# Kernel tuning notes

Measured on AMD Instinct MI355X. Metric: run time of the kernel, lower is better.

The kernel has to match this reference:

```python
import jax, jax.numpy as jnp
import numpy as np
from jax import lax

EPS = 1e-5
TRUNK_C, REG_C, GPOOL_C = 256, 192, 64
B, H, W = 256, 19, 19


def setup_inputs() -> dict:
    key = jax.random.key(0)
    ks = jax.random.split(key, 18)
    def bn_params(k, c):
        k1, k2, k3, k4 = jax.random.split(k, 4)
        return (jax.random.normal(k1, (c,)) * 0.1 + 1.0,   # gamma
                jax.random.normal(k2, (c,)) * 0.1,          # beta
                jax.random.normal(k3, (c,)) * 0.1,          # running mean
                jax.random.uniform(k4, (c,)) * 0.5 + 0.5)   # running var
    bn1_g, bn1_b, bn1_m, bn1_v = bn_params(ks[0], TRUNK_C)
    bn1b_g, bn1b_b, bn1b_m, bn1b_v = bn_params(ks[1], GPOOL_C)
    bn2_g, bn2_b, bn2_m, bn2_v = bn_params(ks[2], REG_C)
    x = jax.random.normal(ks[3], (B, TRUNK_C, H, W), dtype=jnp.float32)
    w1a = jax.random.normal(ks[4], (REG_C, TRUNK_C, 3, 3), dtype=jnp.float32) * (1.0 / np.sqrt(TRUNK_C * 9))
    w1b = jax.random.normal(ks[5], (GPOOL_C, TRUNK_C, 3, 3), dtype=jnp.float32) * (1.0 / np.sqrt(TRUNK_C * 9))
    w_lin = jax.random.normal(ks[6], (REG_C, 3 * GPOOL_C), dtype=jnp.float32) * (1.0 / np.sqrt(3 * GPOOL_C))
    w2 = jax.random.normal(ks[7], (TRUNK_C, REG_C, 3, 3), dtype=jnp.float32) * (1.0 / np.sqrt(REG_C * 9))
    return {
        'x': x, 'bn1_g': bn1_g, 'bn1_b': bn1_b, 'bn1_m': bn1_m, 'bn1_v': bn1_v,
        'w1a': w1a, 'w1b': w1b,
        'bn1b_g': bn1b_g, 'bn1b_b': bn1b_b, 'bn1b_m': bn1b_m, 'bn1b_v': bn1b_v,
        'w_lin': w_lin,
        'bn2_g': bn2_g, 'bn2_b': bn2_b, 'bn2_m': bn2_m, 'bn2_v': bn2_v,
        'w2': w2,
    }


def _bn(x, g, b, m, v):
    # inference batchnorm over channel dim of NCHW
    inv = g / jnp.sqrt(v + EPS)
    return (x - m[:, None, None]) * inv[:, None, None] + b[:, None, None]


def _mish(x):
    return x * jnp.tanh(jax.nn.softplus(x))


def _conv(x, w):
    return lax.conv_general_dilated(x, w, (1, 1), 'SAME',
                                    dimension_numbers=('NCHW', 'OIHW', 'NCHW'))


def _kata_gpool(x):
    # x: [B, C, H, W] -> [B, 3C]: mean, mean*(sqrt(N)-14)/10, max
    b, c, h, w = x.shape
    n = float(h * w)
    sqrt_n = n ** 0.5
    mean = jnp.sum(x, axis=(2, 3)) / n
    max_val = jnp.max(x, axis=(2, 3))
    scaled_mean = mean * ((sqrt_n - 14.0) / 10.0)
    return jnp.concatenate([mean, scaled_mean, max_val], axis=1)


def reference(x, bn1_g, bn1_b, bn1_m, bn1_v, w1a, w1b,
              bn1b_g, bn1b_b, bn1b_m, bn1b_v, w_lin,
              bn2_g, bn2_b, bn2_m, bn2_v, w2):
    out = _mish(_bn(x, bn1_g, bn1_b, bn1_m, bn1_v))
    reg = _conv(out, w1a)                       # [B, REG_C, H, W]
    gp = _conv(out, w1b)                        # [B, GPOOL_C, H, W]
    gp = _mish(_bn(gp, bn1b_g, bn1b_b, bn1b_m, bn1b_v))
    gp_pooled = _kata_gpool(gp)                 # [B, 3*GPOOL_C]
    gp_out = gp_pooled @ w_lin.T                # [B, REG_C]
    reg = reg + gp_out[:, :, None, None]
    out2 = _mish(_bn(reg, bn2_g, bn2_b, bn2_m, bn2_v))
    out2 = _conv(out2, w2)
    return out2 + x
```

## Files before the change

kernel.cpp:

```cpp
#include <hip/hip_runtime.h>
#include <hip/hip_bf16.h>
#include <math.h>


#define BATCH   256
#define TRUNK_C 256
#define REG_C   192
#define GPOOL_C 64
#define HH      19
#define WW      19
#define HW      361
#define PP      441
#define EPS     1e-5f

typedef __hip_bfloat16 bf16;
typedef __attribute__((ext_vector_type(8))) short short8;
typedef __attribute__((ext_vector_type(4))) float floatx4;

__device__ __forceinline__ float b2f(bf16 v) { return __bfloat162float(v); }
__device__ __forceinline__ bf16  f2b(float v) { return __float2bfloat16(v); }

__device__ __forceinline__ float mish_f(float v) {
    if (v > 20.0f) return v;
    float u = __expf(v);
    float n = u * (u + 2.0f);
    return v * __fdividef(n, n + 2.0f);
}

__device__ __forceinline__ void gload_lds16(const void* gsrc, void* lds) {
    __builtin_amdgcn_global_load_lds(
        (const __attribute__((address_space(1))) void*)gsrc,
        (__attribute__((address_space(3))) void*)lds, 16, 0, 0);
}

__global__ void prep_kernel(
    const float* g1, const float* b1, const float* m1, const float* v1,
    const float* g1b, const float* b1b, const float* m1b, const float* v1b,
    const float* g2, const float* b2, const float* m2, const float* v2,
    const float* __restrict__ w1a, const float* __restrict__ w1b,
    const float* __restrict__ w2,
    bf16* __restrict__ w1c_p, bf16* __restrict__ w2_p,
    bf16* __restrict__ act_pad, bf16* __restrict__ reg_pad,
    float* bnbuf)
{
    const int T1  = 16 * 72 * 64 * 8;
    const int T2  = 16 * 54 * 64 * 8;
    const int TW  = T1 + T2;
    const int TBa = BATCH * 80 * 32;
    const int TBr = BATCH * 80 * 24;
    int i = blockIdx.x * blockDim.x + threadIdx.x;
    if (i < TW) {
        if (i < T1) {
            int j = i & 7, lane = (i >> 3) & 63;
            int kc = (i >> 9) % 72, cog = (i >> 9) / 72;
            int co = cog * 16 + (lane & 15);
            int k = kc * 32 + ((lane >> 4) << 3) + j;
            int r = k >> 8, ci = k & 255;
            float v = (co < 192) ? w1a[co * 2304 + ci * 9 + r]
                                 : w1b[(co - 192) * 2304 + ci * 9 + r];
            w1c_p[i] = f2b(v);
        } else {
            int i2 = i - T1;
            int j = i2 & 7, lane = (i2 >> 3) & 63;
            int kc = (i2 >> 9) % 54, cog = (i2 >> 9) / 54;
            int co = cog * 16 + (lane & 15);
            int k = kc * 32 + ((lane >> 4) << 3) + j;
            int r = k / 192, ci = k % 192;
            w2_p[i2] = f2b(w2[co * 1728 + ci * 9 + r]);
        }
    } else if (i < TW + TBa + TBr) {
        int j = i - TW;
        bool isact = j < TBa;
        if (!isact) j -= TBa;
        int nb = isact ? 32 : 24;
        int b = j / (80 * nb);
        int rem = j - b * (80 * nb);
        int e = rem / nb, g = rem - (rem / nb) * nb;
        int pp;
        if (e < 21) pp = e;
        else if (e < 42) pp = 420 + (e - 21);
        else if (e < 61) pp = (e - 41) * 21;
        else pp = (e - 60) * 21 + 20;
        short8 z = {0, 0, 0, 0, 0, 0, 0, 0};
        if (isact) *(short8*)(act_pad + ((size_t)b * PP + pp) * TRUNK_C + g * 8) = z;
        else       *(short8*)(reg_pad + ((size_t)b * PP + pp) * REG_C + g * 8) = z;
    } else {
        int t = i - (TW + TBa + TBr);
        if (t < 256) {
            float s = g1[t] / sqrtf(v1[t] + EPS);
            bnbuf[t] = s;
            bnbuf[256 + t] = b1[t] - m1[t] * s;
        } else if (t < 320) {
            int c = t - 256;
            float s = g1b[c] / sqrtf(v1b[c] + EPS);
            bnbuf[512 + c] = s;
            bnbuf[576 + c] = b1b[c] - m1b[c] * s;
        } else if (t < 512) {
            int c = t - 320;
            float s = g2[c] / sqrtf(v2[c] + EPS);
            bnbuf[640 + c] = s;
            bnbuf[832 + c] = b2[c] - m2[c] * s;
        }
    }
}

__global__ __launch_bounds__(256)
void bn1_mish_t_kernel(const float* __restrict__ x, const float* __restrict__ bnbuf,
                       bf16* __restrict__ act_pad) {
    __shared__ float lds[256][32];
    int pc = blockIdx.x;
    int b  = blockIdx.y;
    int t  = threadIdx.x;
    int p0 = pc * 32;
    int px = t & 31;
#pragma unroll
    for (int it = 0; it < 32; ++it) {
        int ci = it * 8 + (t >> 5);
        int p  = p0 + px;
        float v = 0.0f;
        if (p < HW) v = x[((size_t)b * TRUNK_C + ci) * HW + p];
        v = v * bnbuf[ci] + bnbuf[256 + ci];
        lds[ci][px ^ (ci >> 3)] = mish_f(v);
    }
    __syncthreads();
#pragma unroll
    for (int it = 0; it < 4; ++it) {
        int pl = it * 8 + (t >> 5);
        int p  = p0 + pl;
        if (p >= HW) continue;
        int ch = t & 31;
        short8 vv;
#pragma unroll
        for (int j = 0; j < 8; ++j) {
            bf16 h = f2b(lds[ch * 8 + j][pl ^ ch]);
            short s;
            __builtin_memcpy(&s, &h, 2);
            vv[j] = s;
        }
        int pp = (p / WW + 1) * 21 + (p % WW + 1);
        *(short8*)(act_pad + ((size_t)b * PP + pp) * TRUNK_C + ch * 8) = vv;
    }
}

__device__ __forceinline__ void decode_wg(int wg, int& b, int& mt, int& nh) {
    int g = wg >> 4, r = wg & 15;
    nh = r >> 3;
    int pr = (g << 3) | (r & 7);
    b = pr / 3;
    mt = pr - b * 3;
}

__global__ __launch_bounds__(256, 3)
void conv1_kernel(const bf16* __restrict__ act,
                  const bf16* __restrict__ wfrag,
                  bf16* __restrict__ reg_out,
                  bf16* __restrict__ gp_out,
                  const float* __restrict__ ep_scale, const float* __restrict__ ep_bias) {
    const int CIN = 256, NKC = 72;
    __shared__ __align__(16) bf16 atile[4][128 * 32];
    int b, mt, nh;
    decode_wg(blockIdx.x, b, mt, nh);
    const int t   = threadIdx.x;
    const int w   = t >> 6, lane = t & 63;
    const int mi  = w >> 1, ni = w & 1;
    const int l15 = lane & 15, quad = lane >> 4;

    int row0 = t >> 2;
    int sq   = t & 3;
    int ss   = sq ^ ((row0 >> 1) & 3);
    int sp0  = mt * 128 + row0;      if (sp0 > 360) sp0 = 360;
    int sp1  = mt * 128 + row0 + 64; if (sp1 > 360) sp1 = 360;
    const bf16* sb0 = act + ((size_t)b * PP + (sp0 / WW) * 21 + (sp0 % WW)) * CIN + (ss << 3);
    const bf16* sb1 = act + ((size_t)b * PP + (sp1 / WW) * 21 + (sp1 % WW)) * CIN + (ss << 3);

    const bf16* wb[4];
#pragma unroll
    for (int ns = 0; ns < 4; ++ns)
        wb[ns] = wfrag + ((size_t)(nh * 8 + ni * 4 + ns) * NKC * 64 + lane) * 8;

    int aoff[4];
#pragma unroll
    for (int ms = 0; ms < 4; ++ms) {
        int row = mi * 64 + ms * 16 + l15;
        aoff[ms] = row * 32 + ((quad ^ ((row >> 1) & 3)) << 3);
    }

    auto stage = [&](int buf, int kc) {
        int r = kc >> 3, c = kc & 7;
        int off = ((r / 3) * 21 + (r % 3)) * CIN + (c << 5);
        bf16* dst = &atile[buf][w << 9];
        gload_lds16(sb0 + off, dst);
        gload_lds16(sb1 + off, dst + 2048);
    };

    floatx4 acc[4][4];
#pragma unroll
    for (int i = 0; i < 4; ++i)
#pragma unroll
        for (int j = 0; j < 4; ++j) acc[i][j] = (floatx4){0.f, 0.f, 0.f, 0.f};

    short8 afr[4], bfrA[4], bfrB[4];
    stage(0, 0);
    stage(1, 1);
    asm volatile("" ::: "memory");
#pragma unroll
    for (int ns = 0; ns < 4; ++ns) bfrA[ns] = *(const short8*)(wb[ns]);

    for (int kc = 0; kc < NKC; kc += 2) {
        if (kc == 0) asm volatile("s_waitcnt vmcnt(4)" ::: "memory");
        else         asm volatile("s_waitcnt vmcnt(8)" ::: "memory");
        __builtin_amdgcn_sched_barrier(0);
        __builtin_amdgcn_s_barrier();
        __builtin_amdgcn_sched_barrier(0);
        {
            int s0 = kc + 2; if (s0 > NKC - 1) s0 = NKC - 1;
            int s1 = kc + 3; if (s1 > NKC - 1) s1 = NKC - 1;
            stage((kc + 2) & 3, s0);
            stage((kc + 3) & 3, s1);
        }
        asm volatile("" ::: "memory");
#pragma unroll
        for (int ns = 0; ns < 4; ++ns)
            bfrB[ns] = *(const short8*)(wb[ns] + (size_t)(kc + 1) * 512);
        asm volatile("" ::: "memory");
        {
            const bf16* at = atile[kc & 3];
#pragma unroll
            for (int ms = 0; ms < 4; ++ms)
                afr[ms] = *(const short8*)(at + aoff[ms]);
        }
        __builtin_amdgcn_s_setprio(1);
#pragma unroll
        for (int ms = 0; ms < 4; ++ms)
#pragma unroll
            for (int ns = 0; ns < 4; ++ns)
                acc[ms][ns] = __builtin_amdgcn_mfma_f32_16x16x32_bf16(
                    afr[ms], bfrA[ns], acc[ms][ns], 0, 0, 0);
        __builtin_amdgcn_s_setprio(0);
        {
            int nb = kc + 2; if (nb > NKC - 1) nb = NKC - 1;
#pragma unroll
            for (int ns = 0; ns < 4; ++ns)
                bfrA[ns] = *(const short8*)(wb[ns] + (size_t)nb * 512);
        }
        asm volatile("" ::: "memory");
        {
            const bf16* at = atile[(kc + 1) & 3];
#pragma unroll
            for (int ms = 0; ms < 4; ++ms)
                afr[ms] = *(const short8*)(at + aoff[ms]);
        }
        __builtin_amdgcn_s_setprio(1);
#pragma unroll
        for (int ms = 0; ms < 4; ++ms)
#pragma unroll
            for (int ns = 0; ns < 4; ++ns)
                acc[ms][ns] = __builtin_amdgcn_mfma_f32_16x16x32_bf16(
                    afr[ms], bfrB[ns], acc[ms][ns], 0, 0, 0);
        __builtin_amdgcn_s_setprio(0);
    }

    float scl[4], bia[4];
#pragma unroll
    for (int ns = 0; ns < 4; ++ns) {
        int co = (nh * 8 + ni * 4 + ns) * 16 + l15;
        if (co >= 192) { scl[ns] = ep_scale[co - 192]; bia[ns] = ep_bias[co - 192]; }
    }
#pragma unroll
    for (int ms = 0; ms < 4; ++ms) {
#pragma unroll
        for (int rg = 0; rg < 4; ++rg) {
            int p = mt * 128 + mi * 64 + ms * 16 + quad * 4 + rg;
            if (p > 360) continue;
            size_t ppad = (size_t)b * PP + (p / WW + 1) * 21 + (p % WW + 1);
#pragma unroll
            for (int ns = 0; ns < 4; ++ns) {
                int co = (nh * 8 + ni * 4 + ns) * 16 + l15;
                float v = acc[ms][ns][rg];
                if (co < 192) {
                    reg_out[ppad * REG_C + co] = f2b(v);
                } else {
                    v = mish_f(v * scl[ns] + bia[ns]);
                    gp_out[((size_t)b * HW + p) * GPOOL_C + (co - 192)] = f2b(v);
                }
            }
        }
    }
}

__global__ __launch_bounds__(256, 3)
void conv2_kernel(const bf16* __restrict__ act,
                  const bf16* __restrict__ wfrag,
                  const float* __restrict__ resid,
                  float* __restrict__ out) {
    const int CIN = 192, NKC = 54;
    __shared__ __align__(16) bf16 atile[4][128 * 32];
    int b, mt, nh;
    decode_wg(blockIdx.x, b, mt, nh);
    const int t   = threadIdx.x;
    const int w   = t >> 6, lane = t & 63;
    const int pw  = w >> 1, cw = w & 1;
    const int l15 = lane & 15, quad = lane >> 4;

    int row0 = t >> 2;
    int sq   = t & 3;
    int ss   = sq ^ ((row0 >> 1) & 3);
    int sp0  = mt * 128 + row0;      if (sp0 > 360) sp0 = 360;
    int sp1  = mt * 128 + row0 + 64; if (sp1 > 360) sp1 = 360;
    const bf16* sb0 = act + ((size_t)b * PP + (sp0 / WW) * 21 + (sp0 % WW)) * CIN + (ss << 3);
    const bf16* sb1 = act + ((size_t)b * PP + (sp1 / WW) * 21 + (sp1 % WW)) * CIN + (ss << 3);

    const bf16* wb[4];
#pragma unroll
    for (int ms = 0; ms < 4; ++ms)
        wb[ms] = wfrag + ((size_t)(nh * 8 + cw * 4 + ms) * NKC * 64 + lane) * 8;

    int aoff[4];
#pragma unroll
    for (int ns = 0; ns < 4; ++ns) {
        int row = pw * 64 + ns * 16 + l15;
        aoff[ns] = row * 32 + ((quad ^ ((row >> 1) & 3)) << 3);
    }

    auto stage = [&](int buf, int kc) {
        int r = kc / 6, c = kc % 6;
        int off = ((r / 3) * 21 + (r % 3)) * CIN + (c << 5);
        bf16* dst = &atile[buf][w << 9];
        gload_lds16(sb0 + off, dst);
        gload_lds16(sb1 + off, dst + 2048);
    };

    floatx4 acc[4][4];
#pragma unroll
    for (int i = 0; i < 4; ++i)
#pragma unroll
        for (int j = 0; j < 4; ++j) acc[i][j] = (floatx4){0.f, 0.f, 0.f, 0.f};

    short8 bfa[4], wfrA[4], wfrB[4];
    stage(0, 0);
    stage(1, 1);
    asm volatile("" ::: "memory");
#pragma unroll
    for (int ms = 0; ms < 4; ++ms) wfrA[ms] = *(const short8*)(wb[ms]);

    for (int kc = 0; kc < NKC; kc += 2) {
        if (kc == 0) asm volatile("s_waitcnt vmcnt(4)" ::: "memory");
        else         asm volatile("s_waitcnt vmcnt(8)" ::: "memory");
        __builtin_amdgcn_sched_barrier(0);
        __builtin_amdgcn_s_barrier();
        __builtin_amdgcn_sched_barrier(0);
        {
            int s0 = kc + 2; if (s0 > NKC - 1) s0 = NKC - 1;
            int s1 = kc + 3; if (s1 > NKC - 1) s1 = NKC - 1;
            stage((kc + 2) & 3, s0);
            stage((kc + 3) & 3, s1);
        }
        asm volatile("" ::: "memory");
#pragma unroll
        for (int ms = 0; ms < 4; ++ms)
            wfrB[ms] = *(const short8*)(wb[ms] + (size_t)(kc + 1) * 512);
        asm volatile("" ::: "memory");
        {
            const bf16* at = atile[kc & 3];
#pragma unroll
            for (int ns = 0; ns < 4; ++ns)
                bfa[ns] = *(const short8*)(at + aoff[ns]);
        }
        __builtin_amdgcn_s_setprio(1);
#pragma unroll
        for (int ms = 0; ms < 4; ++ms)
#pragma unroll
            for (int ns = 0; ns < 4; ++ns)
                acc[ms][ns] = __builtin_amdgcn_mfma_f32_16x16x32_bf16(
                    wfrA[ms], bfa[ns], acc[ms][ns], 0, 0, 0);
        __builtin_amdgcn_s_setprio(0);
        {
            int nb = kc + 2; if (nb > NKC - 1) nb = NKC - 1;
#pragma unroll
            for (int ms = 0; ms < 4; ++ms)
                wfrA[ms] = *(const short8*)(wb[ms] + (size_t)nb * 512);
        }
        asm volatile("" ::: "memory");
        {
            const bf16* at = atile[(kc + 1) & 3];
#pragma unroll
            for (int ns = 0; ns < 4; ++ns)
                bfa[ns] = *(const short8*)(at + aoff[ns]);
        }
        __builtin_amdgcn_s_setprio(1);
#pragma unroll
        for (int ms = 0; ms < 4; ++ms)
#pragma unroll
            for (int ns = 0; ns < 4; ++ns)
                acc[ms][ns] = __builtin_amdgcn_mfma_f32_16x16x32_bf16(
                    wfrB[ms], bfa[ns], acc[ms][ns], 0, 0, 0);
        __builtin_amdgcn_s_setprio(0);
    }

#pragma unroll
    for (int ns = 0; ns < 4; ++ns) {
        int p = mt * 128 + pw * 64 + ns * 16 + l15;
        if (p > 360) continue;
#pragma unroll
        for (int ms = 0; ms < 4; ++ms) {
#pragma unroll
            for (int rg = 0; rg < 4; ++rg) {
                int co = (nh * 8 + cw * 4 + ms) * 16 + quad * 4 + rg;
                size_t idx = ((size_t)b * TRUNK_C + co) * HW + p;
                out[idx] = acc[ms][ns][rg] + resid[idx];
            }
        }
    }
}

__global__ __launch_bounds__(256)
void gpool_bn2_kernel(const bf16* __restrict__ gp, const float* __restrict__ w_lin,
                      const float* __restrict__ bnbuf, bf16* __restrict__ reg_pad) {
    __shared__ float ls[4][64], lm[4][64];
    __shared__ float pooled_s[192];
    __shared__ float gob_s[192];
    __shared__ float s2_s[192];
    int b = blockIdx.x;
    int t = threadIdx.x;
    int c = t & 63, sub = t >> 6;
    float s = 0.0f, mx = -1e30f;
    for (int p = sub; p < HW; p += 4) {
        float v = b2f(gp[((size_t)b * HW + p) * GPOOL_C + c]);
        s += v;
        mx = fmaxf(mx, v);
    }
    ls[sub][c] = s; lm[sub][c] = mx;
    __syncthreads();
    if (t < 64) {
        float ss = ls[0][t] + ls[1][t] + ls[2][t] + ls[3][t];
        float mm = fmaxf(fmaxf(lm[0][t], lm[1][t]), fmaxf(lm[2][t], lm[3][t]));
        float mean = ss * (1.0f / 361.0f);
        pooled_s[t] = mean;
        pooled_s[64 + t] = mean * 0.5f;
        pooled_s[128 + t] = mm;
    }
    __syncthreads();
    if (t < 192) {
        const float4* wr4 = (const float4*)(w_lin + t * 192);
        float acc = 0.0f;
#pragma unroll 8
        for (int j = 0; j < 48; ++j) {
            float4 wv = wr4[j];
            acc = fmaf(pooled_s[j * 4 + 0], wv.x, acc);
            acc = fmaf(pooled_s[j * 4 + 1], wv.y, acc);
            acc = fmaf(pooled_s[j * 4 + 2], wv.z, acc);
            acc = fmaf(pooled_s[j * 4 + 3], wv.w, acc);
        }
        float s2 = bnbuf[640 + t];
        s2_s[t]  = s2;
        gob_s[t] = acc * s2 + bnbuf[832 + t];
    }
    __syncthreads();
    for (int i = t; i < HW * 24; i += 256) {
        int p = i / 24, g = i - (i / 24) * 24;
        int pp = (p / WW + 1) * 21 + (p % WW + 1);
        size_t idx = ((size_t)b * PP + pp) * REG_C + g * 8;
        short8 v = *(const short8*)(reg_pad + idx);
        short8 o;
#pragma unroll
        for (int j = 0; j < 8; ++j) {
            int cc = g * 8 + j;
            short sj = v[j];
            bf16 h;
            __builtin_memcpy(&h, &sj, 2);
            float f = b2f(h) * s2_s[cc] + gob_s[cc];
            h = f2b(mish_f(f));
            __builtin_memcpy(&sj, &h, 2);
            o[j] = sj;
        }
        *(short8*)(reg_pad + idx) = o;
    }
}

extern "C" void kernel_launch(void* const* d_in, const int* in_sizes, int n_in,
                              void* d_out, int out_size, void* d_ws, size_t ws_size,
                              hipStream_t stream) {
    const float* x     = (const float*)d_in[0];
    const float* bn1_g = (const float*)d_in[1];
    const float* bn1_b = (const float*)d_in[2];
    const float* bn1_m = (const float*)d_in[3];
    const float* bn1_v = (const float*)d_in[4];
    const float* w1a   = (const float*)d_in[5];
    const float* w1b   = (const float*)d_in[6];
    const float* bn1b_g = (const float*)d_in[7];
    const float* bn1b_b = (const float*)d_in[8];
    const float* bn1b_m = (const float*)d_in[9];
    const float* bn1b_v = (const float*)d_in[10];
    const float* w_lin  = (const float*)d_in[11];
    const float* bn2_g  = (const float*)d_in[12];
    const float* bn2_b  = (const float*)d_in[13];
    const float* bn2_m  = (const float*)d_in[14];
    const float* bn2_v  = (const float*)d_in[15];
    const float* w2     = (const float*)d_in[16];
    float* out = (float*)d_out;

    char* ws = (char*)d_ws;
    size_t off = 0;
    auto alloc = [&](size_t bytes) {
        void* p = ws + off;
        off += (bytes + 255) & ~(size_t)255;
        return p;
    };
    bf16*  act_pad = (bf16*)alloc((size_t)BATCH * PP * TRUNK_C * sizeof(bf16));
    bf16*  reg_pad = (bf16*)alloc((size_t)BATCH * PP * REG_C * sizeof(bf16));
    bf16*  gp      = (bf16*)alloc((size_t)BATCH * HW * GPOOL_C * sizeof(bf16));
    bf16*  w1c_p   = (bf16*)alloc((size_t)16 * 72 * 64 * 8 * sizeof(bf16));
    bf16*  w2_p    = (bf16*)alloc((size_t)16 * 54 * 64 * 8 * sizeof(bf16));
    float* bnbuf   = (float*)alloc(1024 * sizeof(float));
    (void)ws_size;

    {
        const int total = (16 * 72 * 64 * 8) + (16 * 54 * 64 * 8)
                        + BATCH * 80 * 32 + BATCH * 80 * 24 + 512;
        hipLaunchKernelGGL(prep_kernel, dim3((total + 255) / 256), dim3(256), 0, stream,
                           bn1_g, bn1_b, bn1_m, bn1_v,
                           bn1b_g, bn1b_b, bn1b_m, bn1b_v,
                           bn2_g, bn2_b, bn2_m, bn2_v,
                           w1a, w1b, w2, w1c_p, w2_p, act_pad, reg_pad, bnbuf);
    }

    hipLaunchKernelGGL(bn1_mish_t_kernel, dim3(12, BATCH), dim3(256), 0, stream,
                       x, bnbuf, act_pad);

    hipLaunchKernelGGL(conv1_kernel, dim3(1536), dim3(256), 0, stream,
                       act_pad, w1c_p, reg_pad, gp, bnbuf + 512, bnbuf + 576);

    hipLaunchKernelGGL(gpool_bn2_kernel, dim3(BATCH), dim3(256), 0, stream,
                       gp, w_lin, bnbuf, reg_pad);

    hipLaunchKernelGGL(conv2_kernel, dim3(1536), dim3(256), 0, stream,
                       reg_pad, w2_p, x, out);
}
```

Before: 563.8 us.

## Stage conv weights through LDS with triple buffering; split gpool and bn2-mish kernels

Both conv kernels now copy weight fragments into shared memory with async global-to-LDS loads alongside the activation tiles, using a three-deep ring instead of four activation buffers plus register-prefetched weights. The main loop is one k-chunk per iteration with a single wait and barrier. The gpool kernel is split in two: a per-batch pooling+linear kernel writing a small buffer, and a fully parallel elementwise bn2+mish kernel over reg_pad. This is meant to take weight-load latency off the MFMA path and to spread the elementwise pass over many more blocks. The cost is more barriers per k-chunk, extra LDS traffic, and one more kernel launch.

```diff
diff --git a/kernel.cpp b/kernel.cpp
--- a/kernel.cpp
+++ b/kernel.cpp
@@ -157,7 +157,8 @@
                   bf16* __restrict__ gp_out,
                   const float* __restrict__ ep_scale, const float* __restrict__ ep_bias) {
     const int CIN = 256, NKC = 72;
-    __shared__ __align__(16) bf16 atile[4][128 * 32];
+    __shared__ __align__(16) bf16 atile[3][128 * 32];
+    __shared__ __align__(16) bf16 wtile[3][8 * 512];
     int b, mt, nh;
     decode_wg(blockIdx.x, b, mt, nh);
     const int t   = threadIdx.x;
@@ -173,10 +174,8 @@
     const bf16* sb0 = act + ((size_t)b * PP + (sp0 / WW) * 21 + (sp0 % WW)) * CIN + (ss << 3);
     const bf16* sb1 = act + ((size_t)b * PP + (sp1 / WW) * 21 + (sp1 % WW)) * CIN + (ss << 3);
 
-    const bf16* wb[4];
-#pragma unroll
-    for (int ns = 0; ns < 4; ++ns)
-        wb[ns] = wfrag + ((size_t)(nh * 8 + ni * 4 + ns) * NKC * 64 + lane) * 8;
+    const bf16* wsrc0 = wfrag + ((size_t)(nh * 8 + 0 * 4 + w) * NKC) * 512 + lane * 8;
+    const bf16* wsrc1 = wfrag + ((size_t)(nh * 8 + 1 * 4 + w) * NKC) * 512 + lane * 8;
 
     int aoff[4];
 #pragma unroll
@@ -184,13 +183,19 @@
         int row = mi * 64 + ms * 16 + l15;
         aoff[ms] = row * 32 + ((quad ^ ((row >> 1) & 3)) << 3);
     }
+    int boff[4];
+#pragma unroll
+    for (int ns = 0; ns < 4; ++ns)
+        boff[ns] = (ni * 4 + ns) * 512 + lane * 8;
 
     auto stage = [&](int buf, int kc) {
         int r = kc >> 3, c = kc & 7;
         int off = ((r / 3) * 21 + (r % 3)) * CIN + (c << 5);
-        bf16* dst = &atile[buf][w << 9];
-        gload_lds16(sb0 + off, dst);
-        gload_lds16(sb1 + off, dst + 2048);
+        bf16* adst = &atile[buf][w << 9];
+        gload_lds16(sb0 + off, adst);
+        gload_lds16(sb1 + off, adst + 2048);
+        gload_lds16(wsrc0 + (size_t)kc * 512, &wtile[buf][(0 * 4 + w) * 512]);
+        gload_lds16(wsrc1 + (size_t)kc * 512, &wtile[buf][(1 * 4 + w) * 512]);
     };
 
     floatx4 acc[4][4];
@@ -199,35 +204,30 @@
 #pragma unroll
         for (int j = 0; j < 4; ++j) acc[i][j] = (floatx4){0.f, 0.f, 0.f, 0.f};
 
-    short8 afr[4], bfrA[4], bfrB[4];
+    short8 afr[4], bfr[4];
     stage(0, 0);
     stage(1, 1);
-    asm volatile("" ::: "memory");
-#pragma unroll
-    for (int ns = 0; ns < 4; ++ns) bfrA[ns] = *(const short8*)(wb[ns]);
-
-    for (int kc = 0; kc < NKC; kc += 2) {
-        if (kc == 0) asm volatile("s_waitcnt vmcnt(4)" ::: "memory");
-        else         asm volatile("s_waitcnt vmcnt(8)" ::: "memory");
+
+    int rb = 0;
+    for (int kc = 0; kc < NKC; ++kc) {
+        int sbuf = rb + 2; if (sbuf >= 3) sbuf -= 3;
+        int nb   = rb + 1; if (nb >= 3) nb -= 3;
+        asm volatile("s_waitcnt vmcnt(4)" ::: "memory");
         __builtin_amdgcn_sched_barrier(0);
         __builtin_amdgcn_s_barrier();
         __builtin_amdgcn_sched_barrier(0);
         {
-            int s0 = kc + 2; if (s0 > NKC - 1) s0 = NKC - 1;
-            int s1 = kc + 3; if (s1 > NKC - 1) s1 = NKC - 1;
-            stage((kc + 2) & 3, s0);
-            stage((kc + 3) & 3, s1);
-        }
-        asm volatile("" ::: "memory");
-#pragma unroll
-        for (int ns = 0; ns < 4; ++ns)
-            bfrB[ns] = *(const short8*)(wb[ns] + (size_t)(kc + 1) * 512);
+            int s = kc + 2; if (s > NKC - 1) s = NKC - 1;
+            stage(sbuf, s);
+        }
         asm volatile("" ::: "memory");
         {
-            const bf16* at = atile[kc & 3];
-#pragma unroll
-            for (int ms = 0; ms < 4; ++ms)
-                afr[ms] = *(const short8*)(at + aoff[ms]);
+            const bf16* at = &atile[rb][0];
+            const bf16* wt = &wtile[rb][0];
+#pragma unroll
+            for (int ms = 0; ms < 4; ++ms) afr[ms] = *(const short8*)(at + aoff[ms]);
+#pragma unroll
+            for (int ns = 0; ns < 4; ++ns) bfr[ns] = *(const short8*)(wt + boff[ns]);
         }
         __builtin_amdgcn_s_setprio(1);
 #pragma unroll
@@ -235,29 +235,9 @@
 #pragma unroll
             for (int ns = 0; ns < 4; ++ns)
                 acc[ms][ns] = __builtin_amdgcn_mfma_f32_16x16x32_bf16(
-                    afr[ms], bfrA[ns], acc[ms][ns], 0, 0, 0);
+                    afr[ms], bfr[ns], acc[ms][ns], 0, 0, 0);
         __builtin_amdgcn_s_setprio(0);
-        {
-            int nb = kc + 2; if (nb > NKC - 1) nb = NKC - 1;
-#pragma unroll
-            for (int ns = 0; ns < 4; ++ns)
-                bfrA[ns] = *(const short8*)(wb[ns] + (size_t)nb * 512);
-        }
-        asm volatile("" ::: "memory");
-        {
-            const bf16* at = atile[(kc + 1) & 3];
-#pragma unroll
-            for (int ms = 0; ms < 4; ++ms)
-                afr[ms] = *(const short8*)(at + aoff[ms]);
-        }
-        __builtin_amdgcn_s_setprio(1);
-#pragma unroll
-        for (int ms = 0; ms < 4; ++ms)
-#pragma unroll
-            for (int ns = 0; ns < 4; ++ns)
-                acc[ms][ns] = __builtin_amdgcn_mfma_f32_16x16x32_bf16(
-                    afr[ms], bfrB[ns], acc[ms][ns], 0, 0, 0);
-        __builtin_amdgcn_s_setprio(0);
+        rb = nb;
     }
 
     float scl[4], bia[4];
@@ -294,7 +274,8 @@
                   const float* __restrict__ resid,
                   float* __restrict__ out) {
     const int CIN = 192, NKC = 54;
-    __shared__ __align__(16) bf16 atile[4][128 * 32];
+    __shared__ __align__(16) bf16 atile[3][128 * 32];
+    __shared__ __align__(16) bf16 wtile[3][8 * 512];
     int b, mt, nh;
     decode_wg(blockIdx.x, b, mt, nh);
     const int t   = threadIdx.x;
@@ -310,10 +291,8 @@
     const bf16* sb0 = act + ((size_t)b * PP + (sp0 / WW) * 21 + (sp0 % WW)) * CIN + (ss << 3);
     const bf16* sb1 = act + ((size_t)b * PP + (sp1 / WW) * 21 + (sp1 % WW)) * CIN + (ss << 3);
 
-    const bf16* wb[4];
-#pragma unroll
-    for (int ms = 0; ms < 4; ++ms)
-        wb[ms] = wfrag + ((size_t)(nh * 8 + cw * 4 + ms) * NKC * 64 + lane) * 8;
+    const bf16* wsrc0 = wfrag + ((size_t)(nh * 8 + 0 * 4 + w) * NKC) * 512 + lane * 8;
+    const bf16* wsrc1 = wfrag + ((size_t)(nh * 8 + 1 * 4 + w) * NKC) * 512 + lane * 8;
 
     int aoff[4];
 #pragma unroll
@@ -321,13 +300,19 @@
         int row = pw * 64 + ns * 16 + l15;
         aoff[ns] = row * 32 + ((quad ^ ((row >> 1) & 3)) << 3);
     }
+    int woff[4];
+#pragma unroll
+    for (int ms = 0; ms < 4; ++ms)
+        woff[ms] = (cw * 4 + ms) * 512 + lane * 8;
 
     auto stage = [&](int buf, int kc) {
         int r = kc / 6, c = kc % 6;
         int off = ((r / 3) * 21 + (r % 3)) * CIN + (c << 5);
-        bf16* dst = &atile[buf][w << 9];
-        gload_lds16(sb0 + off, dst);
-        gload_lds16(sb1 + off, dst + 2048);
+        bf16* adst = &atile[buf][w << 9];
+        gload_lds16(sb0 + off, adst);
+        gload_lds16(sb1 + off, adst + 2048);
+        gload_lds16(wsrc0 + (size_t)kc * 512, &wtile[buf][(0 * 4 + w) * 512]);
+        gload_lds16(wsrc1 + (size_t)kc * 512, &wtile[buf][(1 * 4 + w) * 512]);
     };
 
     floatx4 acc[4][4];
@@ -336,35 +321,30 @@
 #pragma unroll
         for (int j = 0; j < 4; ++j) acc[i][j] = (floatx4){0.f, 0.f, 0.f, 0.f};
 
-    short8 bfa[4], wfrA[4], wfrB[4];
+    short8 bfa[4], wfr[4];
     stage(0, 0);
     stage(1, 1);
-    asm volatile("" ::: "memory");
-#pragma unroll
-    for (int ms = 0; ms < 4; ++ms) wfrA[ms] = *(const short8*)(wb[ms]);
-
-    for (int kc = 0; kc < NKC; kc += 2) {
-        if (kc == 0) asm volatile("s_waitcnt vmcnt(4)" ::: "memory");
-        else         asm volatile("s_waitcnt vmcnt(8)" ::: "memory");
+
+    int rb = 0;
+    for (int kc = 0; kc < NKC; ++kc) {
+        int sbuf = rb + 2; if (sbuf >= 3) sbuf -= 3;
+        int nb   = rb + 1; if (nb >= 3) nb -= 3;
+        asm volatile("s_waitcnt vmcnt(4)" ::: "memory");
         __builtin_amdgcn_sched_barrier(0);
         __builtin_amdgcn_s_barrier();
         __builtin_amdgcn_sched_barrier(0);
         {
-            int s0 = kc + 2; if (s0 > NKC - 1) s0 = NKC - 1;
-            int s1 = kc + 3; if (s1 > NKC - 1) s1 = NKC - 1;
-            stage((kc + 2) & 3, s0);
-            stage((kc + 3) & 3, s1);
-        }
-        asm volatile("" ::: "memory");
-#pragma unroll
-        for (int ms = 0; ms < 4; ++ms)
-            wfrB[ms] = *(const short8*)(wb[ms] + (size_t)(kc + 1) * 512);
+            int s = kc + 2; if (s > NKC - 1) s = NKC - 1;
+            stage(sbuf, s);
+        }
         asm volatile("" ::: "memory");
         {
-            const bf16* at = atile[kc & 3];
-#pragma unroll
-            for (int ns = 0; ns < 4; ++ns)
-                bfa[ns] = *(const short8*)(at + aoff[ns]);
+            const bf16* at = &atile[rb][0];
+            const bf16* wt = &wtile[rb][0];
+#pragma unroll
+            for (int ns = 0; ns < 4; ++ns) bfa[ns] = *(const short8*)(at + aoff[ns]);
+#pragma unroll
+            for (int ms = 0; ms < 4; ++ms) wfr[ms] = *(const short8*)(wt + woff[ms]);
         }
         __builtin_amdgcn_s_setprio(1);
 #pragma unroll
@@ -372,29 +352,9 @@
 #pragma unroll
             for (int ns = 0; ns < 4; ++ns)
                 acc[ms][ns] = __builtin_amdgcn_mfma_f32_16x16x32_bf16(
-                    wfrA[ms], bfa[ns], acc[ms][ns], 0, 0, 0);
+                    wfr[ms], bfa[ns], acc[ms][ns], 0, 0, 0);
         __builtin_amdgcn_s_setprio(0);
-        {
-            int nb = kc + 2; if (nb > NKC - 1) nb = NKC - 1;
-#pragma unroll
-            for (int ms = 0; ms < 4; ++ms)
-                wfrA[ms] = *(const short8*)(wb[ms] + (size_t)nb * 512);
-        }
-        asm volatile("" ::: "memory");
-        {
-            const bf16* at = atile[(kc + 1) & 3];
-#pragma unroll
-            for (int ns = 0; ns < 4; ++ns)
-                bfa[ns] = *(const short8*)(at + aoff[ns]);
-        }
-        __builtin_amdgcn_s_setprio(1);
-#pragma unroll
-        for (int ms = 0; ms < 4; ++ms)
-#pragma unroll
-            for (int ns = 0; ns < 4; ++ns)
-                acc[ms][ns] = __builtin_amdgcn_mfma_f32_16x16x32_bf16(
-                    wfrB[ms], bfa[ns], acc[ms][ns], 0, 0, 0);
-        __builtin_amdgcn_s_setprio(0);
+        rb = nb;
     }
 
 #pragma unroll
@@ -413,13 +373,10 @@
     }
 }
 
-__global__ __launch_bounds__(256)
-void gpool_bn2_kernel(const bf16* __restrict__ gp, const float* __restrict__ w_lin,
-                      const float* __restrict__ bnbuf, bf16* __restrict__ reg_pad) {
+__global__ void gpool_lin_kernel(const bf16* __restrict__ gp, const float* __restrict__ w_lin,
+                                 const float* __restrict__ bnbuf, float* __restrict__ gob) {
     __shared__ float ls[4][64], lm[4][64];
     __shared__ float pooled_s[192];
-    __shared__ float gob_s[192];
-    __shared__ float s2_s[192];
     int b = blockIdx.x;
     int t = threadIdx.x;
     int c = t & 63, sub = t >> 6;
@@ -451,30 +408,37 @@
             acc = fmaf(pooled_s[j * 4 + 2], wv.z, acc);
             acc = fmaf(pooled_s[j * 4 + 3], wv.w, acc);
         }
-        float s2 = bnbuf[640 + t];
-        s2_s[t]  = s2;
-        gob_s[t] = acc * s2 + bnbuf[832 + t];
-    }
-    __syncthreads();
-    for (int i = t; i < HW * 24; i += 256) {
-        int p = i / 24, g = i - (i / 24) * 24;
-        int pp = (p / WW + 1) * 21 + (p % WW + 1);
-        size_t idx = ((size_t)b * PP + pp) * REG_C + g * 8;
-        short8 v = *(const short8*)(reg_pad + idx);
-        short8 o;
-#pragma unroll
-        for (int j = 0; j < 8; ++j) {
-            int cc = g * 8 + j;
-            short sj = v[j];
-            bf16 h;
-            __builtin_memcpy(&h, &sj, 2);
-            float f = b2f(h) * s2_s[cc] + gob_s[cc];
-            h = f2b(mish_f(f));
-            __builtin_memcpy(&sj, &h, 2);
-            o[j] = sj;
-        }
-        *(short8*)(reg_pad + idx) = o;
-    }
+        gob[b * 192 + t] = acc * bnbuf[640 + t] + bnbuf[832 + t];
+    }
+}
+
+__global__ __launch_bounds__(256)
+void bn2_mish_kernel(bf16* __restrict__ reg_pad, const float* __restrict__ gob,
+                     const float* __restrict__ bnbuf) {
+    const int total = BATCH * HW * 24;
+    int i = blockIdx.x * blockDim.x + threadIdx.x;
+    if (i >= total) return;
+    int g  = i % 24;
+    int bp = i / 24;
+    int p  = bp % HW;
+    int b  = bp / HW;
+    int pp = (p / WW + 1) * 21 + (p % WW + 1);
+    size_t idx = ((size_t)b * PP + pp) * REG_C + g * 8;
+    short8 v = *(const short8*)(reg_pad + idx);
+    const float* go = gob + b * 192 + g * 8;
+    const float* sc = bnbuf + 640 + g * 8;
+    short8 o;
+#pragma unroll
+    for (int j = 0; j < 8; ++j) {
+        short sj = v[j];
+        bf16 h;
+        __builtin_memcpy(&h, &sj, 2);
+        float f = b2f(h) * sc[j] + go[j];
+        h = f2b(mish_f(f));
+        __builtin_memcpy(&sj, &h, 2);
+        o[j] = sj;
+    }
+    *(short8*)(reg_pad + idx) = o;
 }
 
 extern "C" void kernel_launch(void* const* d_in, const int* in_sizes, int n_in,
@@ -511,6 +475,7 @@
     bf16*  gp      = (bf16*)alloc((size_t)BATCH * HW * GPOOL_C * sizeof(bf16));
     bf16*  w1c_p   = (bf16*)alloc((size_t)16 * 72 * 64 * 8 * sizeof(bf16));
     bf16*  w2_p    = (bf16*)alloc((size_t)16 * 54 * 64 * 8 * sizeof(bf16));
+    float* gob     = (float*)alloc((size_t)BATCH * 192 * sizeof(float));
     float* bnbuf   = (float*)alloc(1024 * sizeof(float));
     (void)ws_size;
 
@@ -530,8 +495,14 @@
     hipLaunchKernelGGL(conv1_kernel, dim3(1536), dim3(256), 0, stream,
                        act_pad, w1c_p, reg_pad, gp, bnbuf + 512, bnbuf + 576);
 
-    hipLaunchKernelGGL(gpool_bn2_kernel, dim3(BATCH), dim3(256), 0, stream,
-                       gp, w_lin, bnbuf, reg_pad);
+    hipLaunchKernelGGL(gpool_lin_kernel, dim3(BATCH), dim3(256), 0, stream,
+                       gp, w_lin, bnbuf, gob);
+
+    {
+        int total = BATCH * HW * 24;
+        hipLaunchKernelGGL(bn2_mish_kernel, dim3((total + 255) / 256), dim3(256), 0, stream,
+                           reg_pad, gob, bnbuf);
+    }
 
     hipLaunchKernelGGL(conv2_kernel, dim3(1536), dim3(256), 0, stream,
                        reg_pad, w2_p, x, out);
```

After: 624.5 us. +10.8%, slower.
